# Kernel tuning notes

Measured on AMD Instinct MI355X. Metric: run time of the kernel, lower is better.

## Reference

```python
import jax, jax.numpy as jnp
import numpy as np

B, T, N, D = 8, 64, 512, 128
K = 8            # num_heads
HD = D // K      # per-head dim d = 16
MASK_VAL = -32767.0  # -2**15 + 1, matches torch code
EPS = 1e-6


def layer_norm(x, gamma, beta):
    # torch.std default is unbiased (ddof=1); gamma*(x-mean)/(std+eps)+beta
    mean = x.mean(-1, keepdims=True)
    std = jnp.std(x, axis=-1, keepdims=True, ddof=1)
    return gamma * (x - mean) / (std + EPS) + beta


def setup_inputs() -> dict:
    key = jax.random.key(0)
    ks = jax.random.split(key, 16)
    s = 0.02
    inp = {
        'inputs': jax.random.normal(ks[0], (B, T, N, D), jnp.float32),
        'STE':    jax.random.normal(ks[1], (B, T, N, D), jnp.float32),
        'mask':   1,
        'gamma1': jnp.ones((D,), jnp.float32),
        'beta1':  jnp.zeros((D,), jnp.float32),
        'gamma2': jnp.ones((D,), jnp.float32),
        'beta2':  jnp.zeros((D,), jnp.float32),
        'Wq': jax.random.normal(ks[2], (2 * D, D), jnp.float32) * s,
        'bq': jnp.zeros((D,), jnp.float32),
        'Wk': jax.random.normal(ks[3], (2 * D, D), jnp.float32) * s,
        'bk': jnp.zeros((D,), jnp.float32),
        'Wv': jax.random.normal(ks[4], (2 * D, D), jnp.float32) * s,
        'bv': jnp.zeros((D,), jnp.float32),
        'Wo1': jax.random.normal(ks[5], (D, D), jnp.float32) * s,
        'bo1': jnp.zeros((D,), jnp.float32),
        'Wo2': jax.random.normal(ks[6], (D, D), jnp.float32) * s,
        'bo2': jnp.zeros((D,), jnp.float32),
        'Wf1': jax.random.normal(ks[7], (D, D), jnp.float32) * s,
        'bf1': jnp.zeros((D,), jnp.float32),
        'Wf2': jax.random.normal(ks[8], (D, D), jnp.float32) * s,
        'bf2': jnp.zeros((D,), jnp.float32),
    }
    return inp


def temporal_attention(x_norm, STE, mask, Wq, bq, Wk, bk, Wv, bv, Wo1, bo1, Wo2, bo2):
    b, t, n, dm = x_norm.shape
    X2 = jnp.concatenate([x_norm, STE], axis=-1)              # [B,T,N,2D]
    q = jax.nn.relu(X2 @ Wq + bq).reshape(b, t, n, K, HD)
    k = jax.nn.relu(X2 @ Wk + bk).reshape(b, t, n, K, HD)
    v = jax.nn.relu(X2 @ Wv + bv).reshape(b, t, n, K, HD)
    # split heads on last dim + cat on batch == explicit head axis; attention over time
    scores = jnp.einsum('bqnkd,bpnkd->bknqp', q, k) / jnp.sqrt(jnp.float32(HD))
    if mask:
        tril = jnp.tril(jnp.ones((t, t), bool))               # causal over time steps
        scores = jnp.where(tril, scores, MASK_VAL)
    attn = jax.nn.softmax(scores, axis=-1)                    # [B,K,N,T,T]
    out = jnp.einsum('bknqp,bpnkd->bqnkd', attn, v).reshape(b, t, n, dm)
    return jax.nn.relu(out @ Wo1 + bo1) @ Wo2 + bo2


def reference(inputs, STE, mask, gamma1, beta1, gamma2, beta2,
              Wq, bq, Wk, bk, Wv, bv, Wo1, bo1, Wo2, bo2,
              Wf1, bf1, Wf2, bf2):
    x = inputs
    x_norm = layer_norm(x, gamma1, beta1)
    y = temporal_attention(x_norm, STE, mask, Wq, bq, Wk, bk, Wv, bv,
                           Wo1, bo1, Wo2, bo2)
    x = x + y                                                 # dropout p=0
    x_norm = layer_norm(x, gamma2, beta2)
    # PositionwiseFeedForward 'll': relu after EVERY layer (i < len(layers) is always true)
    h = jax.nn.relu(x_norm @ Wf1 + bf1)
    h = jax.nn.relu(h @ Wf2 + bf2)
    return x + h
```

## Files before the change

### kernel.cpp

```cpp
#include <hip/hip_runtime.h>

#define TT 64
#define NN 512
#define DD 128

typedef __attribute__((ext_vector_type(8))) short bf16x8;
typedef __attribute__((ext_vector_type(4))) float f32x4;

__device__ __forceinline__ unsigned cvtpk(float lo, float hi) {
  unsigned r;
  asm("v_cvt_pk_bf16_f32 %0, %1, %2" : "=v"(r) : "v"(lo), "v"(hi));
  return r;
}

__device__ __forceinline__ float bf2f(unsigned short v) {
  return __uint_as_float((unsigned)v << 16);
}

__device__ __forceinline__ int swz128(int row, int col) {
  return row * 128 + (((col >> 3) ^ (row & 15)) << 3) + (col & 7);
}
__device__ __forceinline__ int swz64(int row, int col) {
  return row * 64 + (((col >> 3) ^ (row & 7)) << 3) + (col & 7);
}

__device__ __forceinline__ void bar() {
  asm volatile("s_waitcnt lgkmcnt(0)" ::: "memory");
  __builtin_amdgcn_s_barrier();
  asm volatile("" ::: "memory");
}

__device__ __forceinline__ float red16(float s) {
  int t;
  t = __builtin_amdgcn_update_dpp(0, __float_as_int(s), 0x121, 0xf, 0xf, false);
  s += __int_as_float(t);
  t = __builtin_amdgcn_update_dpp(0, __float_as_int(s), 0x122, 0xf, 0xf, false);
  s += __int_as_float(t);
  t = __builtin_amdgcn_update_dpp(0, __float_as_int(s), 0x124, 0xf, 0xf, false);
  s += __int_as_float(t);
  t = __builtin_amdgcn_update_dpp(0, __float_as_int(s), 0x128, 0xf, 0xf, false);
  s += __int_as_float(t);
  return s;
}

__global__ void wprep(const float* __restrict__ src, unsigned short* __restrict__ dst,
                      int K, int Nn) {
  int idx = blockIdx.x * 256 + threadIdx.x;
  if (idx >= K * Nn) return;
  int n = idx / K, k = idx - n * K;
  float f = src[k * Nn + n];
  unsigned u = __float_as_uint(f);
  u += 0x7fffu + ((u >> 16) & 1u);
  dst[idx] = (unsigned short)(u >> 16);
}

#define KSCL 0.36067376022224085f

__global__ __launch_bounds__(512, 4)
void attn_head(const float* __restrict__ x_in, const float* __restrict__ ste,
               const float* __restrict__ g1, const float* __restrict__ b1,
               const unsigned short* __restrict__ wqt, const float* __restrict__ bq,
               const unsigned short* __restrict__ wkt, const float* __restrict__ bk,
               const unsigned short* __restrict__ wvt, const float* __restrict__ bv,
               unsigned short* __restrict__ aoG) {
  __shared__ __align__(16) unsigned short smem[32768];

  const int tid = threadIdx.x;
  const int lane = tid & 63;
  const int w  = tid >> 6;
  const int lg = lane >> 4;
  const int li = lane & 15;
  const int hc = w * 16;

  const int blk = blockIdx.x;
  const int b = blk >> 9;
  const int n = blk & 511;
  const int rs = NN * DD;
  const float* xbase = x_in + (b * TT * NN + n) * DD;
  const float* sbase = ste + (b * TT * NN + n) * DD;

  unsigned short* X2s = smem;
  unsigned short* Qb  = smem;
  unsigned short* AOb = smem + 8192;
  unsigned short* Kb  = smem + 16384;
  unsigned short* Vt  = smem + 24576;

  #define SWZ256(row, col) ((row) * 256 + ((((col) >> 3) ^ ((row) & 15)) << 3) + ((col) & 7))

  {
    const int t0 = w * 8 + lg;
    const float* xr0 = xbase + t0 * rs + li * 8;
    const float* xr1 = xbase + (t0 + 4) * rs + li * 8;
    const float* sr0 = sbase + t0 * rs + li * 8;
    const float* sr1 = sbase + (t0 + 4) * rs + li * 8;
    float4 xA0 = *(const float4*)(xr0);
    float4 xB0 = *(const float4*)(xr0 + 4);
    float4 xA1 = *(const float4*)(xr1);
    float4 xB1 = *(const float4*)(xr1 + 4);
    float4 sA0 = *(const float4*)(sr0);
    float4 sB0 = *(const float4*)(sr0 + 4);
    float4 sA1 = *(const float4*)(sr1);
    float4 sB1 = *(const float4*)(sr1 + 4);
    float4 gA = *(const float4*)(g1 + li * 8);
    float4 gB = *(const float4*)(g1 + li * 8 + 4);
    float4 bA = *(const float4*)(b1 + li * 8);
    float4 bB = *(const float4*)(b1 + li * 8 + 4);

    {
      float s1 = xA0.x + xA0.y + xA0.z + xA0.w + xB0.x + xB0.y + xB0.z + xB0.w;
      float s2 = xA0.x * xA0.x + xA0.y * xA0.y + xA0.z * xA0.z + xA0.w * xA0.w +
                 xB0.x * xB0.x + xB0.y * xB0.y + xB0.z * xB0.z + xB0.w * xB0.w;
      s1 = red16(s1); s2 = red16(s2);
      float mean = s1 * (1.0f / 128.0f);
      float var = fmaxf((s2 - s1 * mean) * (1.0f / 127.0f), 0.0f);
      float inv = 1.0f / (sqrtf(var) + 1e-6f);
      unsigned o01 = cvtpk(gA.x * (xA0.x - mean) * inv + bA.x, gA.y * (xA0.y - mean) * inv + bA.y);
      unsigned o23 = cvtpk(gA.z * (xA0.z - mean) * inv + bA.z, gA.w * (xA0.w - mean) * inv + bA.w);
      unsigned o45 = cvtpk(gB.x * (xB0.x - mean) * inv + bB.x, gB.y * (xB0.y - mean) * inv + bB.y);
      unsigned o67 = cvtpk(gB.z * (xB0.z - mean) * inv + bB.z, gB.w * (xB0.w - mean) * inv + bB.w);
      *(uint4*)(X2s + SWZ256(t0, li * 8)) = (uint4){o01, o23, o45, o67};
    }
    {
      float s1 = xA1.x + xA1.y + xA1.z + xA1.w + xB1.x + xB1.y + xB1.z + xB1.w;
      float s2 = xA1.x * xA1.x + xA1.y * xA1.y + xA1.z * xA1.z + xA1.w * xA1.w +
                 xB1.x * xB1.x + xB1.y * xB1.y + xB1.z * xB1.z + xB1.w * xB1.w;
      s1 = red16(s1); s2 = red16(s2);
      float mean = s1 * (1.0f / 128.0f);
      float var = fmaxf((s2 - s1 * mean) * (1.0f / 127.0f), 0.0f);
      float inv = 1.0f / (sqrtf(var) + 1e-6f);
      unsigned o01 = cvtpk(gA.x * (xA1.x - mean) * inv + bA.x, gA.y * (xA1.y - mean) * inv + bA.y);
      unsigned o23 = cvtpk(gA.z * (xA1.z - mean) * inv + bA.z, gA.w * (xA1.w - mean) * inv + bA.w);
      unsigned o45 = cvtpk(gB.x * (xB1.x - mean) * inv + bB.x, gB.y * (xB1.y - mean) * inv + bB.y);
      unsigned o67 = cvtpk(gB.z * (xB1.z - mean) * inv + bB.z, gB.w * (xB1.w - mean) * inv + bB.w);
      *(uint4*)(X2s + SWZ256(t0 + 4, li * 8)) = (uint4){o01, o23, o45, o67};
    }
    *(uint4*)(X2s + SWZ256(t0, 128 + li * 8)) =
        (uint4){cvtpk(sA0.x, sA0.y), cvtpk(sA0.z, sA0.w), cvtpk(sB0.x, sB0.y), cvtpk(sB0.z, sB0.w)};
    *(uint4*)(X2s + SWZ256(t0 + 4, 128 + li * 8)) =
        (uint4){cvtpk(sA1.x, sA1.y), cvtpk(sA1.z, sA1.w), cvtpk(sB1.x, sB1.y), cvtpk(sB1.z, sB1.w)};
  }

  bar();

  f32x4 va[4], ka[4], qa[4];
  #pragma unroll
  for (int rg = 0; rg < 4; ++rg) {
    va[rg] = (f32x4){0, 0, 0, 0};
    ka[rg] = (f32x4){0, 0, 0, 0};
    qa[rg] = (f32x4){0, 0, 0, 0};
  }
  {
    const unsigned short* vB = wvt + hc * 256;
    const unsigned short* kB = wkt + hc * 256;
    const unsigned short* qB = wqt + hc * 256;
    #pragma unroll
    for (int kk = 0; kk < 8; ++kk) {
      bf16x8 bv_ = *(const bf16x8*)(vB + li * 256 + kk * 32 + lg * 8);
      bf16x8 bk_ = *(const bf16x8*)(kB + li * 256 + kk * 32 + lg * 8);
      bf16x8 bq_ = *(const bf16x8*)(qB + li * 256 + kk * 32 + lg * 8);
      #pragma unroll
      for (int rg = 0; rg < 4; ++rg) {
        bf16x8 af = *(const bf16x8*)(X2s + SWZ256(rg * 16 + li, kk * 32 + lg * 8));
        va[rg] = __builtin_amdgcn_mfma_f32_16x16x32_bf16(af, bv_, va[rg], 0, 0, 0);
        ka[rg] = __builtin_amdgcn_mfma_f32_16x16x32_bf16(af, bk_, ka[rg], 0, 0, 0);
        qa[rg] = __builtin_amdgcn_mfma_f32_16x16x32_bf16(af, bq_, qa[rg], 0, 0, 0);
      }
    }
  }

  {
    float bvv = bv[hc + li];
    int d = hc + li;
    #pragma unroll
    for (int rg = 0; rg < 4; ++rg) {
      float v0 = fmaxf(va[rg][0] + bvv, 0.0f);
      float v1 = fmaxf(va[rg][1] + bvv, 0.0f);
      float v2 = fmaxf(va[rg][2] + bvv, 0.0f);
      float v3 = fmaxf(va[rg][3] + bvv, 0.0f);
      uint2 pv; pv.x = cvtpk(v0, v1); pv.y = cvtpk(v2, v3);
      *(uint2*)(Vt + swz64(d, rg * 16 + lg * 4)) = pv;
    }
  }
  {
    float bkv = bk[hc + li];
    int col = hc + li;
    #pragma unroll
    for (int rg = 0; rg < 4; ++rg) {
      float k0 = fmaxf(ka[rg][0] + bkv, 0.0f) * KSCL;
      float k1 = fmaxf(ka[rg][1] + bkv, 0.0f) * KSCL;
      float k2 = fmaxf(ka[rg][2] + bkv, 0.0f) * KSCL;
      float k3 = fmaxf(ka[rg][3] + bkv, 0.0f) * KSCL;
      unsigned p01 = cvtpk(k0, k1), p23 = cvtpk(k2, k3);
      Kb[swz128(rg * 16 + lg * 4 + 0, col)] = (unsigned short)p01;
      Kb[swz128(rg * 16 + lg * 4 + 1, col)] = (unsigned short)(p01 >> 16);
      Kb[swz128(rg * 16 + lg * 4 + 2, col)] = (unsigned short)p23;
      Kb[swz128(rg * 16 + lg * 4 + 3, col)] = (unsigned short)(p23 >> 16);
    }
  }

  bar();

  {
    float bqv = bq[hc + li];
    int col = hc + li;
    #pragma unroll
    for (int rg = 0; rg < 4; ++rg) {
      float v0 = fmaxf(qa[rg][0] + bqv, 0.0f);
      float v1 = fmaxf(qa[rg][1] + bqv, 0.0f);
      float v2 = fmaxf(qa[rg][2] + bqv, 0.0f);
      float v3 = fmaxf(qa[rg][3] + bqv, 0.0f);
      unsigned p01 = cvtpk(v0, v1), p23 = cvtpk(v2, v3);
      Qb[swz128(rg * 16 + lg * 4 + 0, col)] = (unsigned short)p01;
      Qb[swz128(rg * 16 + lg * 4 + 1, col)] = (unsigned short)(p01 >> 16);
      Qb[swz128(rg * 16 + lg * 4 + 2, col)] = (unsigned short)p23;
      Qb[swz128(rg * 16 + lg * 4 + 3, col)] = (unsigned short)(p23 >> 16);
    }
  }

  {
    const bf16x8 zf = (bf16x8){0, 0, 0, 0, 0, 0, 0, 0};
    bf16x8 kf[4], vf[2];
    #pragma unroll
    for (int pt = 0; pt < 4; ++pt)
      kf[pt] = (lg < 2) ? *(const bf16x8*)(Kb + swz128(pt * 16 + li, hc + lg * 8)) : zf;
    #pragma unroll
    for (int ks = 0; ks < 2; ++ks)
      vf[ks] = *(const bf16x8*)(Vt + swz64(hc + li, ks * 32 + lg * 8));

    #pragma unroll
    for (int qt = 0; qt < 4; ++qt) {
      bf16x8 qf = (lg < 2) ? *(const bf16x8*)(Qb + swz128(qt * 16 + li, hc + lg * 8)) : zf;
      f32x4 st[4];
      #pragma unroll
      for (int pt = 0; pt < 4; ++pt)
        if (pt <= qt)
          st[pt] = __builtin_amdgcn_mfma_f32_16x16x32_bf16(kf[pt], qf, (f32x4){0, 0, 0, 0}, 0, 0, 0);

      float ssum = 0.0f;
      unsigned pa[4], pb[4];
      #pragma unroll
      for (int pt = 0; pt < 4; ++pt) {
        if (pt > qt) { pa[pt] = 0; pb[pt] = 0; continue; }
        float e0 = exp2f(st[pt][0]);
        float e1 = exp2f(st[pt][1]);
        float e2 = exp2f(st[pt][2]);
        float e3 = exp2f(st[pt][3]);
        if (pt == qt) {
          e0 = (4 * lg + 0 > li) ? 0.0f : e0;
          e1 = (4 * lg + 1 > li) ? 0.0f : e1;
          e2 = (4 * lg + 2 > li) ? 0.0f : e2;
          e3 = (4 * lg + 3 > li) ? 0.0f : e3;
        }
        ssum += e0 + e1 + e2 + e3;
        pa[pt] = cvtpk(e0, e1);
        pb[pt] = cvtpk(e2, e3);
      }
      ssum += __shfl_xor(ssum, 16, 64);
      ssum += __shfl_xor(ssum, 32, 64);
      float rinv = 1.0f / ssum;

      f32x4 oa = (f32x4){0, 0, 0, 0};
      #pragma unroll
      for (int ks = 0; ks < 2; ++ks) {
        if (ks * 2 > qt) continue;
        unsigned x = pa[2 * ks], y = pa[2 * ks + 1];
        asm("v_permlane32_swap_b32 %0, %1" : "+v"(x), "+v"(y));
        asm("v_permlane16_swap_b32 %0, %1" : "+v"(x), "+v"(y));
        unsigned u2 = pb[2 * ks], v2 = pb[2 * ks + 1];
        asm("v_permlane32_swap_b32 %0, %1" : "+v"(u2), "+v"(v2));
        asm("v_permlane16_swap_b32 %0, %1" : "+v"(u2), "+v"(v2));
        union { unsigned uw[4]; bf16x8 h; } pu;
        pu.uw[0] = x; pu.uw[1] = u2; pu.uw[2] = y; pu.uw[3] = v2;
        oa = __builtin_amdgcn_mfma_f32_16x16x32_bf16(vf[ks], pu.h, oa, 0, 0, 0);
      }
      uint2 ov;
      ov.x = cvtpk(oa[0] * rinv, oa[1] * rinv);
      ov.y = cvtpk(oa[2] * rinv, oa[3] * rinv);
      *(uint2*)(AOb + swz128(qt * 16 + li, hc + lg * 4)) = ov;
    }
  }

  bar();

  #pragma unroll
  for (int pass = 0; pass < 2; ++pass) {
    int t = w * 8 + pass * 4 + lg;
    uint4 v = *(const uint4*)(AOb + swz128(t, li * 8));
    *(uint4*)(aoG + ((b * TT + t) * NN + n) * DD + li * 8) = v;
  }
  #undef SWZ256
}

__global__ __launch_bounds__(512)
void tail_ffn(const unsigned short* __restrict__ aoG, const float* __restrict__ x_in,
              const float* __restrict__ g2, const float* __restrict__ b2,
              const unsigned short* __restrict__ wo1t, const float* __restrict__ bo1,
              const unsigned short* __restrict__ wo2t, const float* __restrict__ bo2,
              const unsigned short* __restrict__ wf1t, const float* __restrict__ bf1,
              const unsigned short* __restrict__ wf2t, const float* __restrict__ bf2,
              float* __restrict__ out) {
  __shared__ __align__(16) unsigned short smem[24576];
  const int tid = threadIdx.x;
  const int lane = tid & 63;
  const int w  = tid >> 6;
  const int lg = lane >> 4;
  const int li = lane & 15;
  const int hc = w * 16;
  const int R0 = blockIdx.x * 64;

  unsigned short* Ar = smem;
  unsigned short* Br = smem + 8192;
  unsigned short* Cr = smem + 16384;

  #pragma unroll
  for (int p = 0; p < 2; ++p) {
    int t = w * 8 + p * 4 + lg;
    uint4 v = *(const uint4*)(aoG + (R0 + t) * DD + li * 8);
    *(uint4*)(Ar + swz128(t, li * 8)) = v;
  }
  bar();

  {
    f32x4 acc[4];
    #pragma unroll
    for (int i = 0; i < 4; ++i) acc[i] = (f32x4){0, 0, 0, 0};
    #pragma unroll
    for (int kk = 0; kk < 4; ++kk) {
      bf16x8 bc = *(const bf16x8*)(wo1t + (hc + li) * 128 + kk * 32 + lg * 8);
      #pragma unroll
      for (int rg = 0; rg < 4; ++rg) {
        bf16x8 af = *(const bf16x8*)(Ar + swz128(rg * 16 + li, kk * 32 + lg * 8));
        acc[rg] = __builtin_amdgcn_mfma_f32_16x16x32_bf16(af, bc, acc[rg], 0, 0, 0);
      }
    }
    float bvv = bo1[hc + li];
    int col = hc + li;
    #pragma unroll
    for (int rg = 0; rg < 4; ++rg) {
      unsigned p01 = cvtpk(fmaxf(acc[rg][0] + bvv, 0.0f), fmaxf(acc[rg][1] + bvv, 0.0f));
      unsigned p23 = cvtpk(fmaxf(acc[rg][2] + bvv, 0.0f), fmaxf(acc[rg][3] + bvv, 0.0f));
      Br[swz128(rg * 16 + lg * 4 + 0, col)] = (unsigned short)p01;
      Br[swz128(rg * 16 + lg * 4 + 1, col)] = (unsigned short)(p01 >> 16);
      Br[swz128(rg * 16 + lg * 4 + 2, col)] = (unsigned short)p23;
      Br[swz128(rg * 16 + lg * 4 + 3, col)] = (unsigned short)(p23 >> 16);
    }
  }
  bar();

  {
    f32x4 acc[4];
    #pragma unroll
    for (int i = 0; i < 4; ++i) acc[i] = (f32x4){0, 0, 0, 0};
    #pragma unroll
    for (int kk = 0; kk < 4; ++kk) {
      bf16x8 bc = *(const bf16x8*)(wo2t + (hc + li) * 128 + kk * 32 + lg * 8);
      #pragma unroll
      for (int rg = 0; rg < 4; ++rg) {
        bf16x8 af = *(const bf16x8*)(Br + swz128(rg * 16 + li, kk * 32 + lg * 8));
        acc[rg] = __builtin_amdgcn_mfma_f32_16x16x32_bf16(af, bc, acc[rg], 0, 0, 0);
      }
    }
    float bvv = bo2[hc + li];
    int col = hc + li;
    #pragma unroll
    for (int rg = 0; rg < 4; ++rg) {
      float x0 = x_in[(R0 + rg * 16 + lg * 4 + 0) * DD + col];
      float x1 = x_in[(R0 + rg * 16 + lg * 4 + 1) * DD + col];
      float x2v = x_in[(R0 + rg * 16 + lg * 4 + 2) * DD + col];
      float x3 = x_in[(R0 + rg * 16 + lg * 4 + 3) * DD + col];
      unsigned p01 = cvtpk(acc[rg][0] + bvv + x0, acc[rg][1] + bvv + x1);
      unsigned p23 = cvtpk(acc[rg][2] + bvv + x2v, acc[rg][3] + bvv + x3);
      Cr[swz128(rg * 16 + lg * 4 + 0, col)] = (unsigned short)p01;
      Cr[swz128(rg * 16 + lg * 4 + 1, col)] = (unsigned short)(p01 >> 16);
      Cr[swz128(rg * 16 + lg * 4 + 2, col)] = (unsigned short)p23;
      Cr[swz128(rg * 16 + lg * 4 + 3, col)] = (unsigned short)(p23 >> 16);
    }
  }
  bar();

  {
    float4 gA = *(const float4*)(g2 + li * 8);
    float4 gB = *(const float4*)(g2 + li * 8 + 4);
    float4 bA = *(const float4*)(b2 + li * 8);
    float4 bB = *(const float4*)(b2 + li * 8 + 4);
    #pragma unroll
    for (int p = 0; p < 2; ++p) {
      int t = w * 8 + p * 4 + lg;
      uint4 v = *(const uint4*)(Cr + swz128(t, li * 8));
      float f0 = bf2f((unsigned short)v.x),  f1 = bf2f((unsigned short)(v.x >> 16));
      float f2v = bf2f((unsigned short)v.y), f3 = bf2f((unsigned short)(v.y >> 16));
      float f4 = bf2f((unsigned short)v.z),  f5 = bf2f((unsigned short)(v.z >> 16));
      float f6 = bf2f((unsigned short)v.w),  f7 = bf2f((unsigned short)(v.w >> 16));
      float s1 = f0 + f1 + f2v + f3 + f4 + f5 + f6 + f7;
      float s2 = f0 * f0 + f1 * f1 + f2v * f2v + f3 * f3 + f4 * f4 + f5 * f5 + f6 * f6 + f7 * f7;
      s1 = red16(s1); s2 = red16(s2);
      float mean = s1 * (1.0f / 128.0f);
      float var = fmaxf((s2 - s1 * mean) * (1.0f / 127.0f), 0.0f);
      float iv = 1.0f / (sqrtf(var) + 1e-6f);
      unsigned o01 = cvtpk(gA.x * (f0 - mean) * iv + bA.x, gA.y * (f1 - mean) * iv + bA.y);
      unsigned o23 = cvtpk(gA.z * (f2v - mean) * iv + bA.z, gA.w * (f3 - mean) * iv + bA.w);
      unsigned o45 = cvtpk(gB.x * (f4 - mean) * iv + bB.x, gB.y * (f5 - mean) * iv + bB.y);
      unsigned o67 = cvtpk(gB.z * (f6 - mean) * iv + bB.z, gB.w * (f7 - mean) * iv + bB.w);
      *(uint4*)(Ar + swz128(t, li * 8)) = (uint4){o01, o23, o45, o67};
    }
  }
  bar();

  {
    f32x4 acc[4];
    #pragma unroll
    for (int i = 0; i < 4; ++i) acc[i] = (f32x4){0, 0, 0, 0};
    #pragma unroll
    for (int kk = 0; kk < 4; ++kk) {
      bf16x8 bc = *(const bf16x8*)(wf1t + (hc + li) * 128 + kk * 32 + lg * 8);
      #pragma unroll
      for (int rg = 0; rg < 4; ++rg) {
        bf16x8 af = *(const bf16x8*)(Ar + swz128(rg * 16 + li, kk * 32 + lg * 8));
        acc[rg] = __builtin_amdgcn_mfma_f32_16x16x32_bf16(af, bc, acc[rg], 0, 0, 0);
      }
    }
    float bvv = bf1[hc + li];
    int col = hc + li;
    #pragma unroll
    for (int rg = 0; rg < 4; ++rg) {
      unsigned p01 = cvtpk(fmaxf(acc[rg][0] + bvv, 0.0f), fmaxf(acc[rg][1] + bvv, 0.0f));
      unsigned p23 = cvtpk(fmaxf(acc[rg][2] + bvv, 0.0f), fmaxf(acc[rg][3] + bvv, 0.0f));
      Br[swz128(rg * 16 + lg * 4 + 0, col)] = (unsigned short)p01;
      Br[swz128(rg * 16 + lg * 4 + 1, col)] = (unsigned short)(p01 >> 16);
      Br[swz128(rg * 16 + lg * 4 + 2, col)] = (unsigned short)p23;
      Br[swz128(rg * 16 + lg * 4 + 3, col)] = (unsigned short)(p23 >> 16);
    }
  }
  bar();

  {
    f32x4 acc[4];
    #pragma unroll
    for (int i = 0; i < 4; ++i) acc[i] = (f32x4){0, 0, 0, 0};
    #pragma unroll
    for (int kk = 0; kk < 4; ++kk) {
      bf16x8 bc = *(const bf16x8*)(wf2t + (hc + li) * 128 + kk * 32 + lg * 8);
      #pragma unroll
      for (int rg = 0; rg < 4; ++rg) {
        bf16x8 af = *(const bf16x8*)(Br + swz128(rg * 16 + li, kk * 32 + lg * 8));
        acc[rg] = __builtin_amdgcn_mfma_f32_16x16x32_bf16(af, bc, acc[rg], 0, 0, 0);
      }
    }
    float bvv = bf2[hc + li];
    int col = hc + li;
    #pragma unroll
    for (int rg = 0; rg < 4; ++rg) {
      #pragma unroll
      for (int r = 0; r < 4; ++r) {
        int row = rg * 16 + lg * 4 + r;
        float x2v = bf2f(Cr[swz128(row, col)]);
        out[(R0 + row) * DD + col] = x2v + fmaxf(acc[rg][r] + bvv, 0.0f);
      }
    }
  }
}

extern "C" void kernel_launch(void* const* d_in, const int* in_sizes, int n_in,
                              void* d_out, int out_size, void* d_ws, size_t ws_size,
                              hipStream_t stream) {
  const float* x   = (const float*)d_in[0];
  const float* ste = (const float*)d_in[1];
  const float* g1 = (const float*)d_in[3];
  const float* b1 = (const float*)d_in[4];
  const float* g2 = (const float*)d_in[5];
  const float* b2 = (const float*)d_in[6];
  const float* Wq = (const float*)d_in[7];   const float* bq  = (const float*)d_in[8];
  const float* Wk = (const float*)d_in[9];   const float* bk  = (const float*)d_in[10];
  const float* Wv = (const float*)d_in[11];  const float* bv  = (const float*)d_in[12];
  const float* Wo1 = (const float*)d_in[13]; const float* bo1 = (const float*)d_in[14];
  const float* Wo2 = (const float*)d_in[15]; const float* bo2 = (const float*)d_in[16];
  const float* Wf1 = (const float*)d_in[17]; const float* bf1 = (const float*)d_in[18];
  const float* Wf2 = (const float*)d_in[19]; const float* bf2 = (const float*)d_in[20];
  float* out = (float*)d_out;

  unsigned short* wsu = (unsigned short*)d_ws;
  unsigned short* wq_t  = wsu;
  unsigned short* wk_t  = wsu + 32768;
  unsigned short* wv_t  = wsu + 65536;
  unsigned short* wo1_t = wsu + 98304;
  unsigned short* wo2_t = wsu + 114688;
  unsigned short* wf1_t = wsu + 131072;
  unsigned short* wf2_t = wsu + 147456;
  unsigned short* ao    = wsu + 163840;

  hipLaunchKernelGGL(wprep, dim3(128), dim3(256), 0, stream, Wq, wq_t, 256, 128);
  hipLaunchKernelGGL(wprep, dim3(128), dim3(256), 0, stream, Wk, wk_t, 256, 128);
  hipLaunchKernelGGL(wprep, dim3(128), dim3(256), 0, stream, Wv, wv_t, 256, 128);
  hipLaunchKernelGGL(wprep, dim3(64), dim3(256), 0, stream, Wo1, wo1_t, 128, 128);
  hipLaunchKernelGGL(wprep, dim3(64), dim3(256), 0, stream, Wo2, wo2_t, 128, 128);
  hipLaunchKernelGGL(wprep, dim3(64), dim3(256), 0, stream, Wf1, wf1_t, 128, 128);
  hipLaunchKernelGGL(wprep, dim3(64), dim3(256), 0, stream, Wf2, wf2_t, 128, 128);

  hipLaunchKernelGGL(attn_head, dim3(8 * NN), dim3(512), 0, stream,
                     x, ste, g1, b1, wq_t, bq, wk_t, bk, wv_t, bv, ao);
  hipLaunchKernelGGL(tail_ffn, dim3(8 * TT * NN / 64), dim3(512), 0, stream,
                     ao, x, g2, b2, wo1_t, bo1, wo2_t, bo2,
                     wf1_t, bf1, wf2_t, bf2, out);
}
```

Before: 280.6 us.

## Fuse attention and output/FFN tail into a single kernel per (b,n) block

Merges the attention kernel and the tail FFN kernel so each block processes a 64-timestep column for one (b,n) and applies Wo1/Wo2, layernorm and the FFN directly from the attention output in shared memory. This removes the bf16 global round-trip of the attention output and one kernel launch. In exchange, the tail's reads of x and writes of out are now strided by N*D per time step instead of contiguous rows, which may hurt coalescing. The tail also inherits the attention kernel's register and LDS budget under launch_bounds(512,4).

```diff
diff --git a/kernel.cpp b/kernel.cpp
--- a/kernel.cpp
+++ b/kernel.cpp
@@ -57,12 +57,17 @@
 #define KSCL 0.36067376022224085f
 
 __global__ __launch_bounds__(512, 4)
-void attn_head(const float* __restrict__ x_in, const float* __restrict__ ste,
-               const float* __restrict__ g1, const float* __restrict__ b1,
-               const unsigned short* __restrict__ wqt, const float* __restrict__ bq,
-               const unsigned short* __restrict__ wkt, const float* __restrict__ bk,
-               const unsigned short* __restrict__ wvt, const float* __restrict__ bv,
-               unsigned short* __restrict__ aoG) {
+void fused_layer(const float* __restrict__ x_in, const float* __restrict__ ste,
+                 const float* __restrict__ g1, const float* __restrict__ b1,
+                 const float* __restrict__ g2, const float* __restrict__ b2,
+                 const unsigned short* __restrict__ wqt, const float* __restrict__ bq,
+                 const unsigned short* __restrict__ wkt, const float* __restrict__ bk,
+                 const unsigned short* __restrict__ wvt, const float* __restrict__ bv,
+                 const unsigned short* __restrict__ wo1t, const float* __restrict__ bo1,
+                 const unsigned short* __restrict__ wo2t, const float* __restrict__ bo2,
+                 const unsigned short* __restrict__ wf1t, const float* __restrict__ bf1,
+                 const unsigned short* __restrict__ wf2t, const float* __restrict__ bf2,
+                 float* __restrict__ out) {
   __shared__ __align__(16) unsigned short smem[32768];
 
   const int tid = threadIdx.x;
@@ -81,9 +86,12 @@
 
   unsigned short* X2s = smem;
   unsigned short* Qb  = smem;
+  unsigned short* Ar  = smem;
   unsigned short* AOb = smem + 8192;
   unsigned short* Kb  = smem + 16384;
+  unsigned short* Br  = smem + 16384;
   unsigned short* Vt  = smem + 24576;
+  unsigned short* Cr  = smem + 24576;
 
   #define SWZ256(row, col) ((row) * 256 + ((((col) >> 3) ^ ((row) & 15)) << 3) + ((col) & 7))
 
@@ -282,44 +290,6 @@
 
   bar();
 
-  #pragma unroll
-  for (int pass = 0; pass < 2; ++pass) {
-    int t = w * 8 + pass * 4 + lg;
-    uint4 v = *(const uint4*)(AOb + swz128(t, li * 8));
-    *(uint4*)(aoG + ((b * TT + t) * NN + n) * DD + li * 8) = v;
-  }
-  #undef SWZ256
-}
-
-__global__ __launch_bounds__(512)
-void tail_ffn(const unsigned short* __restrict__ aoG, const float* __restrict__ x_in,
-              const float* __restrict__ g2, const float* __restrict__ b2,
-              const unsigned short* __restrict__ wo1t, const float* __restrict__ bo1,
-              const unsigned short* __restrict__ wo2t, const float* __restrict__ bo2,
-              const unsigned short* __restrict__ wf1t, const float* __restrict__ bf1,
-              const unsigned short* __restrict__ wf2t, const float* __restrict__ bf2,
-              float* __restrict__ out) {
-  __shared__ __align__(16) unsigned short smem[24576];
-  const int tid = threadIdx.x;
-  const int lane = tid & 63;
-  const int w  = tid >> 6;
-  const int lg = lane >> 4;
-  const int li = lane & 15;
-  const int hc = w * 16;
-  const int R0 = blockIdx.x * 64;
-
-  unsigned short* Ar = smem;
-  unsigned short* Br = smem + 8192;
-  unsigned short* Cr = smem + 16384;
-
-  #pragma unroll
-  for (int p = 0; p < 2; ++p) {
-    int t = w * 8 + p * 4 + lg;
-    uint4 v = *(const uint4*)(aoG + (R0 + t) * DD + li * 8);
-    *(uint4*)(Ar + swz128(t, li * 8)) = v;
-  }
-  bar();
-
   {
     f32x4 acc[4];
     #pragma unroll
@@ -329,7 +299,7 @@
       bf16x8 bc = *(const bf16x8*)(wo1t + (hc + li) * 128 + kk * 32 + lg * 8);
       #pragma unroll
       for (int rg = 0; rg < 4; ++rg) {
-        bf16x8 af = *(const bf16x8*)(Ar + swz128(rg * 16 + li, kk * 32 + lg * 8));
+        bf16x8 af = *(const bf16x8*)(AOb + swz128(rg * 16 + li, kk * 32 + lg * 8));
         acc[rg] = __builtin_amdgcn_mfma_f32_16x16x32_bf16(af, bc, acc[rg], 0, 0, 0);
       }
     }
@@ -364,10 +334,10 @@
     int col = hc + li;
     #pragma unroll
     for (int rg = 0; rg < 4; ++rg) {
-      float x0 = x_in[(R0 + rg * 16 + lg * 4 + 0) * DD + col];
-      float x1 = x_in[(R0 + rg * 16 + lg * 4 + 1) * DD + col];
-      float x2v = x_in[(R0 + rg * 16 + lg * 4 + 2) * DD + col];
-      float x3 = x_in[(R0 + rg * 16 + lg * 4 + 3) * DD + col];
+      float x0 = xbase[(rg * 16 + lg * 4 + 0) * rs + col];
+      float x1 = xbase[(rg * 16 + lg * 4 + 1) * rs + col];
+      float x2v = xbase[(rg * 16 + lg * 4 + 2) * rs + col];
+      float x3 = xbase[(rg * 16 + lg * 4 + 3) * rs + col];
       unsigned p01 = cvtpk(acc[rg][0] + bvv + x0, acc[rg][1] + bvv + x1);
       unsigned p23 = cvtpk(acc[rg][2] + bvv + x2v, acc[rg][3] + bvv + x3);
       Cr[swz128(rg * 16 + lg * 4 + 0, col)] = (unsigned short)p01;
@@ -446,6 +416,7 @@
         acc[rg] = __builtin_amdgcn_mfma_f32_16x16x32_bf16(af, bc, acc[rg], 0, 0, 0);
       }
     }
+    float* obase = out + (b * TT * NN + n) * DD;
     float bvv = bf2[hc + li];
     int col = hc + li;
     #pragma unroll
@@ -454,10 +425,11 @@
       for (int r = 0; r < 4; ++r) {
         int row = rg * 16 + lg * 4 + r;
         float x2v = bf2f(Cr[swz128(row, col)]);
-        out[(R0 + row) * DD + col] = x2v + fmaxf(acc[rg][r] + bvv, 0.0f);
-      }
-    }
-  }
+        obase[row * rs + col] = x2v + fmaxf(acc[rg][r] + bvv, 0.0f);
+      }
+    }
+  }
+  #undef SWZ256
 }
 
 extern "C" void kernel_launch(void* const* d_in, const int* in_sizes, int n_in,
@@ -486,7 +458,6 @@
   unsigned short* wo2_t = wsu + 114688;
   unsigned short* wf1_t = wsu + 131072;
   unsigned short* wf2_t = wsu + 147456;
-  unsigned short* ao    = wsu + 163840;
 
   hipLaunchKernelGGL(wprep, dim3(128), dim3(256), 0, stream, Wq, wq_t, 256, 128);
   hipLaunchKernelGGL(wprep, dim3(128), dim3(256), 0, stream, Wk, wk_t, 256, 128);
@@ -496,9 +467,9 @@
   hipLaunchKernelGGL(wprep, dim3(64), dim3(256), 0, stream, Wf1, wf1_t, 128, 128);
   hipLaunchKernelGGL(wprep, dim3(64), dim3(256), 0, stream, Wf2, wf2_t, 128, 128);
 
-  hipLaunchKernelGGL(attn_head, dim3(8 * NN), dim3(512), 0, stream,
-                     x, ste, g1, b1, wq_t, bq, wk_t, bk, wv_t, bv, ao);
-  hipLaunchKernelGGL(tail_ffn, dim3(8 * TT * NN / 64), dim3(512), 0, stream,
-                     ao, x, g2, b2, wo1_t, bo1, wo2_t, bo2,
+  hipLaunchKernelGGL(fused_layer, dim3(8 * NN), dim3(512), 0, stream,
+                     x, ste, g1, b1, g2, b2,
+                     wq_t, bq, wk_t, bk, wv_t, bv,
+                     wo1_t, bo1, wo2_t, bo2,
                      wf1_t, bf1, wf2_t, bf2, out);
 }
```

Result: faster. 249.3 us (-11.2%).
